# Optimization experiments

Hardware: AMD Instinct MI355X
Metric: run time of the kernel (lower is better)

Reference implementation:

```python
import jax, jax.numpy as jnp
import numpy as np

NUM_LABELS = 4
MEMO_SIZE = 512
EMBED = 512
BATCH = 16384


def setup_inputs() -> dict:
    key = jax.random.key(0)
    ks = jax.random.split(key, 6)
    B, D, M, C = BATCH, EMBED, MEMO_SIZE, NUM_LABELS
    logits = jax.random.normal(ks[0], (B, C), dtype=jnp.float32)
    text_embeds = jax.random.normal(ks[1], (B, D), dtype=jnp.float32)
    vision_embeds = jax.random.normal(ks[2], (B, D), dtype=jnp.float32)
    # full memory bank: entropy sorted ascending (invariant maintained by the module)
    entropy_memo = jnp.sort(jax.random.uniform(ks[3], (C, M), dtype=jnp.float32), axis=-1)
    text_memo = jax.random.normal(ks[4], (C, M, D), dtype=jnp.float32)
    vision_memo = jax.random.normal(ks[5], (C, M, D), dtype=jnp.float32)
    return {
        "logits": logits,
        "text_embeds": text_embeds,
        "vision_embeds": vision_embeds,
        "entropy_memo": entropy_memo,
        "text_memo": text_memo,
        "vision_memo": vision_memo,
    }


def reference(logits, text_embeds, vision_embeds, entropy_memo, text_memo, vision_memo):
    C, M = entropy_memo.shape
    pred = jax.nn.softmax(logits, axis=-1)                      # [B,C]
    log_pred = jax.nn.log_softmax(logits, axis=-1)
    entropy = -jnp.sum(pred * log_pred, axis=-1)                # [B]
    pseudo_y = jnp.argmax(pred, axis=-1)                        # [B]

    # --- write(): per-label sorted merge of batch items into the memory bank ---
    # Bank is full (ptr == M), so fill_size == M for every label. Items whose
    # pseudo label differs are masked to +inf entropy so they never enter the
    # kept top-M, reproducing the boolean-mask selection with fixed shapes.
    labels = jnp.arange(C)
    batch_ent = jnp.where(pseudo_y[None, :] == labels[:, None], entropy[None, :], jnp.inf)  # [C,B]

    def update_one(ent_memo_l, text_memo_l, vis_memo_l, batch_ent_l):
        cat_ent = jnp.concatenate([ent_memo_l, batch_ent_l])                 # [M+B]
        order = jnp.argsort(cat_ent)[:M]                                     # keep M lowest entropies
        new_text = jnp.concatenate([text_memo_l, text_embeds], axis=0)[order]   # [M,D]
        new_vis = jnp.concatenate([vis_memo_l, vision_embeds], axis=0)[order]   # [M,D]
        return cat_ent[order], new_text, new_vis

    new_ent, new_text_memo, new_vision_memo = jax.vmap(update_one)(
        entropy_memo, text_memo, vision_memo, batch_ent)

    # --- memo lookup: einsum('bd,cmd->bmc').sum(1) == b,d x (sum_m c,d)^T ---
    cosin_text = jnp.einsum('bd,cd->bc', text_embeds, new_text_memo.sum(axis=1))  # [B,C]
    ct = cosin_text
    # NOTE: the original code uses cosin_text for BOTH combines (cosin_vision is dead code);
    # we faithfully reproduce that.
    text_combine = jnp.stack([ct[:, 0] + ct[:, 2], ct[:, 1] + ct[:, 3]], axis=1)    # [B,2]
    vision_combine = jnp.stack([ct[:, 0] + ct[:, 1], ct[:, 2] + ct[:, 3]], axis=1)  # [B,2]
    memo_text_pred = jax.nn.softmax(text_combine, axis=-1)
    memo_vision_pred = jax.nn.softmax(vision_combine, axis=-1)
    memo_pred = jnp.concatenate(
        [memo_text_pred * memo_vision_pred[:, 0:1],
         memo_text_pred * memo_vision_pred[:, 1:2]], axis=1)                        # [B,4]
    return memo_pred, pred, entropy
```

## Files before the change

kernel.cpp:

```cpp
#include <hip/hip_runtime.h>

#define B 16384
#define C 4
#define M 512
#define D 512
#define NSEG 64
#define QSCALE 16777216.0f
#define BCAP_G 2048
#define BCAP_S 1024

__device__ inline unsigned posbits(float e)
{
    unsigned b = __float_as_uint(e);
    return (b == 0x80000000u) ? 0u : b;
}
__device__ inline int binOfBits(unsigned bits)
{
    float e = __uint_as_float(bits);
    float s = fminf(fmaxf(e * 12000000.0f, 0.0f), 16777215.0f);
    return (int)((unsigned)s >> 16);
}

__global__ __launch_bounds__(256) void k1_stats(
    const float* __restrict__ logits,
    const float* __restrict__ ent_memo,
    float* __restrict__ out,
    int* __restrict__ blockCnt,
    uint2* __restrict__ candList,
    unsigned long long* __restrict__ SQ,
    unsigned* __restrict__ hist_part,
    int* __restrict__ bnumG)
{
    __shared__ int wscan[4];
    __shared__ int lh[1024];
    const int tid = threadIdx.x, blk = blockIdx.x;
    const int gid = blk * 256 + tid;
    const int lane = tid & 63, wv = tid >> 6;

    for (int i = tid; i < 1024; i += 256) lh[i] = 0;

    float4 l = *reinterpret_cast<const float4*>(logits + (size_t)gid * 4);
    float m = l.x; int idx = 0;
    if (l.y > m) { m = l.y; idx = 1; }
    if (l.z > m) { m = l.z; idx = 2; }
    if (l.w > m) { m = l.w; idx = 3; }
    float e0 = expf(l.x - m), e1 = expf(l.y - m), e2 = expf(l.z - m), e3 = expf(l.w - m);
    float s = e0 + e1 + e2 + e3;
    float inv = 1.0f / s;
    float p0 = e0 * inv, p1 = e1 * inv, p2 = e2 * inv, p3 = e3 * inv;
    float lse = logf(s);
    float ent = -(p0 * (l.x - m - lse) + p1 * (l.y - m - lse)
                + p2 * (l.z - m - lse) + p3 * (l.w - m - lse));
    float4 pr = { p0, p1, p2, p3 };
    *reinterpret_cast<float4*>(out + (size_t)B * 4 + (size_t)gid * 4) = pr;
    out[(size_t)B * 8 + gid] = ent;

    if (gid < C * M) SQ[gid] = 0ULL;
    if (gid == 0) *bnumG = 0;

    float amax = ent_memo[(idx << 9) + M - 1];
    bool flag = ent < amax;
    unsigned bits = posbits(ent);
    __syncthreads();

    if (flag) atomicAdd(&lh[(idx << 8) | binOfBits(bits)], 1);
    if (blk < 8) {
        unsigned mb = posbits(ent_memo[gid]);
        atomicAdd(&lh[((gid >> 9) << 8) | binOfBits(mb)], 1);
    }

    unsigned long long mask = __ballot(flag);
    int prefix = __popcll(mask & ((1ull << lane) - 1ull));
    if (lane == 0) wscan[wv] = __popcll(mask);
    __syncthreads();
    int base = 0;
    for (int w = 0; w < wv; w++) base += wscan[w];
    if (flag)
        candList[blk * 256 + base + prefix] =
            make_uint2(bits, ((unsigned)idx << 14) | (unsigned)gid);
    if (tid == 0)
        blockCnt[blk] = wscan[0] + wscan[1] + wscan[2] + wscan[3];

    for (int i = tid; i < 512; i += 256)
        hist_part[blk * 512 + i] = (unsigned)lh[2 * i] | ((unsigned)lh[2 * i + 1] << 16);
}

__global__ __launch_bounds__(256) void kT_extract(
    const int* __restrict__ blockCnt,
    const uint2* __restrict__ candList,
    const float* __restrict__ ent_memo,
    const unsigned* __restrict__ hist_part,
    int* __restrict__ mremG,
    int* __restrict__ bnumG,
    unsigned long long* __restrict__ bkeysG,
    int* __restrict__ blabsG)
{
    __shared__ int hist_s[1024];
    __shared__ int betaS[4], mremS[4];
    const int x = blockIdx.x, tid = threadIdx.x;
    const int lane = tid & 63, sg = tid >> 6;

    {
        unsigned a0 = 0u, a1 = 0u;
        for (int sb = 0; sb < NSEG; sb += 8) {
            unsigned v0[8], v1[8];
            #pragma unroll
            for (int u = 0; u < 8; u++) {
                v0[u] = hist_part[(sb + u) * 512 + tid];
                v1[u] = hist_part[(sb + u) * 512 + 256 + tid];
            }
            #pragma unroll
            for (int u = 0; u < 8; u++) { a0 += v0[u]; a1 += v1[u]; }
        }
        hist_s[2 * tid]           = (int)(a0 & 0xFFFFu);
        hist_s[2 * tid + 1]       = (int)(a0 >> 16);
        hist_s[512 + 2 * tid]     = (int)(a1 & 0xFFFFu);
        hist_s[512 + 2 * tid + 1] = (int)(a1 >> 16);
    }
    __syncthreads();

    if (sg < 4) {
        int b0 = hist_s[(sg << 8) | (lane * 4 + 0)];
        int b1 = hist_s[(sg << 8) | (lane * 4 + 1)];
        int b2 = hist_s[(sg << 8) | (lane * 4 + 2)];
        int b3 = hist_s[(sg << 8) | (lane * 4 + 3)];
        int loc = b0 + b1 + b2 + b3;
        int scan = loc;
        #pragma unroll
        for (int off = 1; off < 64; off <<= 1) {
            int n = __shfl_up(scan, off, 64);
            if (lane >= off) scan += n;
        }
        int excl = scan - loc;
        int c0 = excl + b0, c1 = c0 + b1, c2 = c1 + b2, c3 = c2 + b3;
        if (excl < M && c3 >= M) {
            int beta, mrem;
            if (c0 >= M)      { beta = lane * 4 + 0; mrem = M - excl; }
            else if (c1 >= M) { beta = lane * 4 + 1; mrem = M - c0; }
            else if (c2 >= M) { beta = lane * 4 + 2; mrem = M - c1; }
            else              { beta = lane * 4 + 3; mrem = M - c2; }
            betaS[sg] = beta; mremS[sg] = mrem;
        }
    }
    __syncthreads();
    if (x == 0 && tid < 4) mremG[tid] = mremS[tid];

    if (x < NSEG) {
        uint2 v = candList[x * 256 + tid];
        int lab = (int)((v.y >> 14) & 3);
        if (tid < blockCnt[x] && binOfBits(v.x) == betaS[lab]) {
            int id = atomicAdd(bnumG, 1);
            if (id < BCAP_G) {
                bkeysG[id] = ((unsigned long long)v.x << 15)
                           | (unsigned)(512 + (v.y & 0x3FFF));
                blabsG[id] = lab;
            }
        }
    } else {
        int i = (x - NSEG) * 256 + tid;
        unsigned bits = posbits(ent_memo[i]);
        int lab = i >> 9;
        if (binOfBits(bits) == betaS[lab]) {
            int id = atomicAdd(bnumG, 1);
            if (id < BCAP_G) {
                bkeysG[id] = ((unsigned long long)bits << 15) | (unsigned)(i & (M - 1));
                blabsG[id] = lab;
            }
        }
    }
}

__global__ __launch_bounds__(256) void kB_acc(
    const int* __restrict__ blockCnt,
    const uint2* __restrict__ candList,
    const float* __restrict__ ent_memo,
    const int* __restrict__ mremG,
    const int* __restrict__ bnumG,
    const unsigned long long* __restrict__ bkeysG,
    const int* __restrict__ blabsG,
    const float* __restrict__ text_memo,
    const float* __restrict__ text_embeds,
    unsigned long long* __restrict__ SQ)
{
    __shared__ unsigned long long bkeys[BCAP_S];
    __shared__ int blabs[BCAP_S];
    __shared__ int mremS[4];
    __shared__ unsigned long long TkeyS[4];
    __shared__ int meta[256];

    const int x = blockIdx.x, tid = threadIdx.x;
    const int col0 = (x & 7) << 6;
    const int lane = tid & 63, sg = tid >> 6;

    int nb = *bnumG; if (nb > BCAP_S) nb = BCAP_S;
    if (tid < 4) { mremS[tid] = mremG[tid]; TkeyS[tid] = ~0ULL; }
    for (int i = tid; i < nb; i += 256) { bkeys[i] = bkeysG[i]; blabs[i] = blabsG[i]; }
    __syncthreads();
    for (int t = tid; t < nb; t += 256) {
        unsigned long long k = bkeys[t]; int l = blabs[t];
        int r = 0;
        for (int j = 0; j < nb; j++)
            if (blabs[j] == l && bkeys[j] < k) r++;
        if (r == mremS[l] - 1) TkeyS[l] = k;
    }
    __syncthreads();

    if (x < 512) {
        const int seg = x >> 3;
        const int cnt = blockCnt[seg];
        {
            uint2 v = candList[(seg << 8) + tid];
            int lab = (int)((v.y >> 14) & 3);
            unsigned long long key = ((unsigned long long)v.x << 15)
                                   | (unsigned)(512 + (v.y & 0x3FFF));
            bool kept = (tid < cnt) && (key <= TkeyS[lab]);
            meta[tid] = kept ? (int)((unsigned)lab | 4u | ((v.y & 0x3FFF) << 3)) : 0;
        }
        __syncthreads();
        float a0 = 0.f, a1 = 0.f, a2 = 0.f, a3 = 0.f;
        #pragma unroll
        for (int kb = 0; kb < 8; kb++) {
            int mts[8]; float vvs[8];
            #pragma unroll
            for (int u = 0; u < 8; u++)
                mts[u] = meta[(((kb << 3) | u) << 2) | sg];
            #pragma unroll
            for (int u = 0; u < 8; u++)
                vvs[u] = text_embeds[(size_t)(mts[u] >> 3) * D + col0 + lane];
            #pragma unroll
            for (int u = 0; u < 8; u++) {
                bool kept = (mts[u] & 4) != 0;
                int lb = mts[u] & 3;
                float vv = vvs[u];
                a0 += (kept && lb == 0) ? vv : 0.f;
                a1 += (kept && lb == 1) ? vv : 0.f;
                a2 += (kept && lb == 2) ? vv : 0.f;
                a3 += (kept && lb == 3) ? vv : 0.f;
            }
        }
        __shared__ float red[4][4][64];
        red[sg][0][lane] = a0; red[sg][1][lane] = a1;
        red[sg][2][lane] = a2; red[sg][3][lane] = a3;
        __syncthreads();
        float t = ((red[0][sg][lane] + red[1][sg][lane])
                 + red[2][sg][lane]) + red[3][sg][lane];
        long long q = llrintf(t * QSCALE);
        atomicAdd(&SQ[(sg << 9) + col0 + lane], (unsigned long long)q);
    } else {
        const int g = (x - 512) >> 3;
        const int c = g >> 1;
        const int base = g << 8;
        {
            int i = base + tid;
            unsigned bits = posbits(ent_memo[i]);
            unsigned long long key = ((unsigned long long)bits << 15)
                                   | (unsigned)(i & (M - 1));
            meta[tid] = (key <= TkeyS[c]) ? 1 : 0;
        }
        __syncthreads();
        float a = 0.f;
        #pragma unroll
        for (int kb = 0; kb < 8; kb++) {
            float vvs[8];
            #pragma unroll
            for (int u = 0; u < 8; u++)
                vvs[u] = text_memo[(size_t)(base + ((((kb << 3) | u) << 2) | sg)) * D + col0 + lane];
            #pragma unroll
            for (int u = 0; u < 8; u++)
                a += meta[(((kb << 3) | u) << 2) | sg] ? vvs[u] : 0.f;
        }
        __shared__ float redm[4][64];
        redm[sg][lane] = a;
        __syncthreads();
        if (tid < 64) {
            float t = ((redm[0][tid] + redm[1][tid]) + redm[2][tid]) + redm[3][tid];
            long long q = llrintf(t * QSCALE);
            atomicAdd(&SQ[(c << 9) + col0 + tid], (unsigned long long)q);
        }
    }
}

__global__ __launch_bounds__(256) void kC_cosin(
    const unsigned long long* __restrict__ SQ,
    const float* __restrict__ text_embeds,
    float* __restrict__ out)
{
    const int tid = threadIdx.x;
    const int wave = tid >> 6, lane = tid & 63;
    const float sc = 1.0f / QSCALE;
    float s0[8], s1[8], s2[8], s3[8];
    #pragma unroll
    for (int j = 0; j < 8; j++) {
        s0[j] = (float)(long long)SQ[0 * 512 + lane * 8 + j] * sc;
        s1[j] = (float)(long long)SQ[1 * 512 + lane * 8 + j] * sc;
        s2[j] = (float)(long long)SQ[2 * 512 + lane * 8 + j] * sc;
        s3[j] = (float)(long long)SQ[3 * 512 + lane * 8 + j] * sc;
    }
    for (int r4 = 0; r4 < 4; r4++) {
        int b = blockIdx.x * 16 + wave * 4 + r4;
        const float4* te4 = reinterpret_cast<const float4*>(text_embeds + (size_t)b * D);
        float4 t0 = te4[lane * 2], t1 = te4[lane * 2 + 1];
        float te[8] = { t0.x, t0.y, t0.z, t0.w, t1.x, t1.y, t1.z, t1.w };
        float c0 = 0.f, c1 = 0.f, c2 = 0.f, c3 = 0.f;
        #pragma unroll
        for (int j = 0; j < 8; j++) {
            c0 += te[j] * s0[j];
            c1 += te[j] * s1[j];
            c2 += te[j] * s2[j];
            c3 += te[j] * s3[j];
        }
        for (int off = 32; off; off >>= 1) {
            c0 += __shfl_down(c0, off, 64);
            c1 += __shfl_down(c1, off, 64);
            c2 += __shfl_down(c2, off, 64);
            c3 += __shfl_down(c3, off, 64);
        }
        if (lane == 0) {
            float t0c = c0 + c2, t1c = c1 + c3;
            float v0c = c0 + c1, v1c = c2 + c3;
            float tm = fmaxf(t0c, t1c);
            float te0 = expf(t0c - tm), te1 = expf(t1c - tm);
            float ts = te0 + te1;
            float mt0 = te0 / ts, mt1 = te1 / ts;
            float vm = fmaxf(v0c, v1c);
            float ve0 = expf(v0c - vm), ve1 = expf(v1c - vm);
            float vs = ve0 + ve1;
            float mv0 = ve0 / vs, mv1 = ve1 / vs;
            float4 o = { mt0 * mv0, mt1 * mv0, mt0 * mv1, mt1 * mv1 };
            *reinterpret_cast<float4*>(out + (size_t)b * 4) = o;
        }
    }
}

extern "C" void kernel_launch(void* const* d_in, const int* in_sizes, int n_in,
                              void* d_out, int out_size, void* d_ws, size_t ws_size,
                              hipStream_t stream)
{
    (void)in_sizes; (void)n_in; (void)out_size; (void)ws_size;
    const float* logits      = (const float*)d_in[0];
    const float* text_embeds = (const float*)d_in[1];
    const float* ent_memo    = (const float*)d_in[3];
    const float* text_memo   = (const float*)d_in[4];
    float* out = (float*)d_out;
    char* ws = (char*)d_ws;

    int*   blockCnt = (int*)(ws + 0);
    uint2* candList = (uint2*)(ws + 256);
    unsigned long long* SQ = (unsigned long long*)(ws + 131328);
    unsigned* hist_part = (unsigned*)(ws + 147712);
    int* mremG = (int*)(ws + 278784);
    int* bnumG = (int*)(ws + 279040);
    unsigned long long* bkeysG = (unsigned long long*)(ws + 279296);
    int* blabsG = (int*)(ws + 295680);

    k1_stats<<<NSEG, 256, 0, stream>>>(logits, ent_memo, out, blockCnt,
                                       candList, SQ, hist_part, bnumG);
    kT_extract<<<NSEG + 8, 256, 0, stream>>>(blockCnt, candList, ent_memo,
                                             hist_part, mremG, bnumG,
                                             bkeysG, blabsG);
    kB_acc<<<576, 256, 0, stream>>>(blockCnt, candList, ent_memo,
                                    mremG, bnumG, bkeysG, blabsG,
                                    text_memo, text_embeds, SQ);
    kC_cosin<<<1024, 256, 0, stream>>>(SQ, text_embeds, out);
}
```

Before: 36.73 us.

## Hoist boundary rank into single-block kernel and split accumulation blocks in half

The O(nb^2) boundary-key rank computation, previously repeated redundantly in every one of the 576 accumulation blocks, moves into a separate one-block kernel that writes the threshold keys to workspace. The accumulation kernel then reads those four keys and runs with twice as many blocks, each covering 128 rows instead of 256, to raise parallelism. The cost is an extra kernel launch on the serial path and twice as many atomic adds into the accumulator.

```diff
diff --git a/kernel.cpp b/kernel.cpp
--- a/kernel.cpp
+++ b/kernel.cpp
@@ -170,27 +170,18 @@
     }
 }
 
-__global__ __launch_bounds__(256) void kB_acc(
-    const int* __restrict__ blockCnt,
-    const uint2* __restrict__ candList,
-    const float* __restrict__ ent_memo,
+__global__ __launch_bounds__(256) void kT2_rank(
     const int* __restrict__ mremG,
     const int* __restrict__ bnumG,
     const unsigned long long* __restrict__ bkeysG,
     const int* __restrict__ blabsG,
-    const float* __restrict__ text_memo,
-    const float* __restrict__ text_embeds,
-    unsigned long long* __restrict__ SQ)
+    unsigned long long* __restrict__ TkeyG)
 {
     __shared__ unsigned long long bkeys[BCAP_S];
     __shared__ int blabs[BCAP_S];
     __shared__ int mremS[4];
     __shared__ unsigned long long TkeyS[4];
-    __shared__ int meta[256];
-
-    const int x = blockIdx.x, tid = threadIdx.x;
-    const int col0 = (x & 7) << 6;
-    const int lane = tid & 63, sg = tid >> 6;
+    const int tid = threadIdx.x;
 
     int nb = *bnumG; if (nb > BCAP_S) nb = BCAP_S;
     if (tid < 4) { mremS[tid] = mremG[tid]; TkeyS[tid] = ~0ULL; }
@@ -204,22 +195,45 @@
         if (r == mremS[l] - 1) TkeyS[l] = k;
     }
     __syncthreads();
-
-    if (x < 512) {
-        const int seg = x >> 3;
-        const int cnt = blockCnt[seg];
-        {
-            uint2 v = candList[(seg << 8) + tid];
+    if (tid < 4) TkeyG[tid] = TkeyS[tid];
+}
+
+__global__ __launch_bounds__(256) void kB_acc(
+    const int* __restrict__ blockCnt,
+    const uint2* __restrict__ candList,
+    const float* __restrict__ ent_memo,
+    const unsigned long long* __restrict__ TkeyG,
+    const float* __restrict__ text_memo,
+    const float* __restrict__ text_embeds,
+    unsigned long long* __restrict__ SQ)
+{
+    __shared__ int meta[128];
+    __shared__ unsigned long long TkeyS[4];
+    __shared__ float red[4][4][64];
+    const int x = blockIdx.x, tid = threadIdx.x;
+    const int lane = tid & 63, sg = tid >> 6;
+
+    if (tid < 4) TkeyS[tid] = TkeyG[tid];
+    __syncthreads();
+
+    if (x < 1024) {
+        const int seg = x >> 4;
+        const int h = (x >> 3) & 1;
+        const int col0 = (x & 7) << 6;
+        const int sbase = h << 7;
+        if (tid < 128) {
+            int slot = sbase + tid;
+            uint2 v = candList[(seg << 8) + slot];
             int lab = (int)((v.y >> 14) & 3);
             unsigned long long key = ((unsigned long long)v.x << 15)
                                    | (unsigned)(512 + (v.y & 0x3FFF));
-            bool kept = (tid < cnt) && (key <= TkeyS[lab]);
+            bool kept = (slot < blockCnt[seg]) && (key <= TkeyS[lab]);
             meta[tid] = kept ? (int)((unsigned)lab | 4u | ((v.y & 0x3FFF) << 3)) : 0;
         }
         __syncthreads();
         float a0 = 0.f, a1 = 0.f, a2 = 0.f, a3 = 0.f;
         #pragma unroll
-        for (int kb = 0; kb < 8; kb++) {
+        for (int kb = 0; kb < 4; kb++) {
             int mts[8]; float vvs[8];
             #pragma unroll
             for (int u = 0; u < 8; u++)
@@ -238,20 +252,24 @@
                 a3 += (kept && lb == 3) ? vv : 0.f;
             }
         }
-        __shared__ float red[4][4][64];
         red[sg][0][lane] = a0; red[sg][1][lane] = a1;
         red[sg][2][lane] = a2; red[sg][3][lane] = a3;
         __syncthreads();
-        float t = ((red[0][sg][lane] + red[1][sg][lane])
-                 + red[2][sg][lane]) + red[3][sg][lane];
-        long long q = llrintf(t * QSCALE);
-        atomicAdd(&SQ[(sg << 9) + col0 + lane], (unsigned long long)q);
+        {
+            int lab = tid >> 6, ln = tid & 63;
+            float t = ((red[0][lab][ln] + red[1][lab][ln])
+                     + red[2][lab][ln]) + red[3][lab][ln];
+            long long q = llrintf(t * QSCALE);
+            atomicAdd(&SQ[(lab << 9) + col0 + ln], (unsigned long long)q);
+        }
     } else {
-        const int g = (x - 512) >> 3;
-        const int c = g >> 1;
-        const int base = g << 8;
-        {
-            int i = base + tid;
+        const int xm = x - 1024;
+        const int hg = xm >> 3;
+        const int col0 = (xm & 7) << 6;
+        const int c = hg >> 2;
+        const int rbase = hg << 7;
+        if (tid < 128) {
+            int i = rbase + tid;
             unsigned bits = posbits(ent_memo[i]);
             unsigned long long key = ((unsigned long long)bits << 15)
                                    | (unsigned)(i & (M - 1));
@@ -260,20 +278,20 @@
         __syncthreads();
         float a = 0.f;
         #pragma unroll
-        for (int kb = 0; kb < 8; kb++) {
+        for (int kb = 0; kb < 4; kb++) {
             float vvs[8];
             #pragma unroll
             for (int u = 0; u < 8; u++)
-                vvs[u] = text_memo[(size_t)(base + ((((kb << 3) | u) << 2) | sg)) * D + col0 + lane];
+                vvs[u] = text_memo[(size_t)(rbase + ((((kb << 3) | u) << 2) | sg)) * D + col0 + lane];
             #pragma unroll
             for (int u = 0; u < 8; u++)
                 a += meta[(((kb << 3) | u) << 2) | sg] ? vvs[u] : 0.f;
         }
-        __shared__ float redm[4][64];
-        redm[sg][lane] = a;
+        red[sg][0][lane] = a;
         __syncthreads();
         if (tid < 64) {
-            float t = ((redm[0][tid] + redm[1][tid]) + redm[2][tid]) + redm[3][tid];
+            float t = ((red[0][0][tid] + red[1][0][tid])
+                     + red[2][0][tid]) + red[3][0][tid];
             long long q = llrintf(t * QSCALE);
             atomicAdd(&SQ[(c << 9) + col0 + tid], (unsigned long long)q);
         }
@@ -352,14 +370,15 @@
     int* bnumG = (int*)(ws + 279040);
     unsigned long long* bkeysG = (unsigned long long*)(ws + 279296);
     int* blabsG = (int*)(ws + 295680);
+    unsigned long long* TkeyG = (unsigned long long*)(ws + 303872);
 
     k1_stats<<<NSEG, 256, 0, stream>>>(logits, ent_memo, out, blockCnt,
                                        candList, SQ, hist_part, bnumG);
     kT_extract<<<NSEG + 8, 256, 0, stream>>>(blockCnt, candList, ent_memo,
                                              hist_part, mremG, bnumG,
                                              bkeysG, blabsG);
-    kB_acc<<<576, 256, 0, stream>>>(blockCnt, candList, ent_memo,
-                                    mremG, bnumG, bkeysG, blabsG,
-                                    text_memo, text_embeds, SQ);
+    kT2_rank<<<1, 256, 0, stream>>>(mremG, bnumG, bkeysG, blabsG, TkeyG);
+    kB_acc<<<1152, 256, 0, stream>>>(blockCnt, candList, ent_memo, TkeyG,
+                                     text_memo, text_embeds, SQ);
     kC_cosin<<<1024, 256, 0, stream>>>(SQ, text_embeds, out);
 }
```

Result: slower. 38.32 us (+4.3%).
